# Kernel optimization log

Measured on AMD Instinct MI355X. Metric: run time of the kernel, lower is better.

Reference implementation:

```python
import jax, jax.numpy as jnp
import numpy as np

N, D, NUM_CLASSES = 4096, 512, 128
MARGIN = 0.3


def setup_inputs() -> dict:
    key = jax.random.key(0)
    k1, k2 = jax.random.split(key)
    embeddings = jax.random.normal(k1, (N, D), dtype=jnp.float32)
    labels = jax.random.randint(k2, (N,), 0, NUM_CLASSES, dtype=jnp.int64)
    return {"embeddings": embeddings, "labels": labels}


def _batch_hard_triplet(embeddings, labels, margin):
    # L2-normalize rows (torch F.normalize: x / max(||x||, eps))
    norm = jnp.linalg.norm(embeddings, axis=1, keepdims=True)
    e = embeddings / jnp.maximum(norm, 1e-12)
    n = e.shape[0]
    # Pairwise Euclidean distance via Gram matrix; ||a-b||^2 = 2 - 2 a.b for unit vectors
    gram = e @ e.T                                   # [N, N]
    sq = jnp.clip(2.0 - 2.0 * gram, 0.0, None)
    # safe sqrt: zero (and exactly-equal) pairs get distance 0 with zero gradient
    nz = sq > 0
    dist = jnp.where(nz, jnp.sqrt(jnp.where(nz, sq, 1.0)), 0.0)  # [N, N]

    same = labels[:, None] == labels[None, :]        # [N, N] bool
    eye = jnp.eye(n, dtype=bool)
    pos_mask = same & ~eye                           # positives excluding self
    neg_mask = ~same

    # hardest positive (row max over positives), hardest negative (row min over negatives)
    dist_ap = jnp.max(jnp.where(pos_mask, dist, -jnp.inf), axis=1)  # [N]
    dist_an = jnp.min(jnp.where(neg_mask, dist, jnp.inf), axis=1)   # [N]

    valid = jnp.any(pos_mask, axis=1) & jnp.any(neg_mask, axis=1)   # rows kept by torch loop
    per_row = jax.nn.relu(dist_ap - dist_an + margin)
    num_valid = jnp.sum(valid)
    loss_sum = jnp.sum(jnp.where(valid, per_row, 0.0))
    return jnp.where(num_valid > 0, loss_sum / jnp.maximum(num_valid, 1), 0.0)


def reference(embeddings, labels):
    return _batch_hard_triplet(embeddings, labels, MARGIN)
```

## Files before the change

### kernel.cpp

```cpp
#include <hip/hip_runtime.h>
#include <hip/hip_bf16.h>
#include <stdint.h>


#define NROW 4096
#define DIM  512
#define NCLS 128
#define MARGIN 0.3f
#define BT 128
#define BK 32

typedef __attribute__((ext_vector_type(8))) __bf16 bf16x8;
typedef __attribute__((ext_vector_type(4))) float  f32x4;

__device__ __forceinline__ unsigned enc(float f) {
    unsigned u = __float_as_uint(f);
    return (u & 0x80000000u) ? ~u : (u | 0x80000000u);
}
__device__ __forceinline__ float dec(unsigned e) {
    return (e & 0x80000000u) ? __uint_as_float(e & 0x7fffffffu)
                             : __uint_as_float(~e);
}

__device__ __forceinline__ unsigned short f2bf(float f) {
    __hip_bfloat16 h = __float2bfloat16(f);
    return *reinterpret_cast<unsigned short*>(&h);
}

__device__ __forceinline__ void async_copy16(const void* g, void* l) {
    __builtin_amdgcn_global_load_lds(
        (const __attribute__((address_space(1))) unsigned int*)g,
        (__attribute__((address_space(3))) unsigned int*)l,
        16, 0, 0);
}

__global__ void tl_init(unsigned* __restrict__ posArr, unsigned* __restrict__ negArr,
                        int* __restrict__ cnt) {
    int t = blockIdx.x * blockDim.x + threadIdx.x;
    if (t < NROW) { posArr[t] = 0xFFFFFFFFu; negArr[t] = 0u; }
    if (t < NCLS) cnt[t] = 0;
}

__global__ void tl_norm(const float* __restrict__ E, const int* __restrict__ labels,
                        __hip_bfloat16* __restrict__ Ebf, int* __restrict__ cnt) {
    int wave = threadIdx.x >> 6;
    int lane = threadIdx.x & 63;
    int row  = blockIdx.x * 4 + wave;

    const float4* src = (const float4*)(E + (size_t)row * DIM);
    float4 v0 = src[lane];
    float4 v1 = src[lane + 64];
    float ss = v0.x*v0.x + v0.y*v0.y + v0.z*v0.z + v0.w*v0.w
             + v1.x*v1.x + v1.y*v1.y + v1.z*v1.z + v1.w*v1.w;
    #pragma unroll
    for (int m = 32; m >= 1; m >>= 1) ss += __shfl_xor(ss, m);
    float inv = 1.0f / fmaxf(sqrtf(ss), 1e-12f);

    ushort4 o0, o1;
    o0.x = f2bf(v0.x * inv); o0.y = f2bf(v0.y * inv);
    o0.z = f2bf(v0.z * inv); o0.w = f2bf(v0.w * inv);
    o1.x = f2bf(v1.x * inv); o1.y = f2bf(v1.y * inv);
    o1.z = f2bf(v1.z * inv); o1.w = f2bf(v1.w * inv);
    ushort4* dst = (ushort4*)(Ebf + (size_t)row * DIM);
    dst[lane]      = o0;
    dst[lane + 64] = o1;

    if (lane == 0) atomicAdd(&cnt[labels[row]], 1);
}

__global__ void tl_gram(const __hip_bfloat16* __restrict__ Ebf,
                        const int* __restrict__ labels,
                        unsigned* __restrict__ posArr,
                        unsigned* __restrict__ negArr) {
    __shared__ __align__(16) __hip_bfloat16 At[BT * BK];
    __shared__ __align__(16) __hip_bfloat16 Bt[BT * BK];
    __shared__ int rowLab[BT];
    __shared__ int colLab[BT];

    const int tid  = threadIdx.x;
    const int wave = tid >> 6;
    const int lane = tid & 63;
    const int quad = lane >> 4;
    const int l16  = lane & 15;
    const int wr   = wave >> 1;
    const int wc   = wave & 1;
    const int tileI = blockIdx.y * BT;
    const int tileJ = blockIdx.x * BT;

    if (tid < BT) rowLab[tid] = labels[tileI + tid];
    else          colLab[tid - BT] = labels[tileJ + (tid - BT)];

    const int sRow = wave * 32 + (lane >> 2);
    const int sK   = (lane & 3) * 8;
    const __hip_bfloat16* gA = Ebf + (size_t)(tileI + sRow) * DIM + sK;
    const __hip_bfloat16* gB = Ebf + (size_t)(tileJ + sRow) * DIM + sK;
    __hip_bfloat16* lA0 = &At[(wave * 2 + 0) * 512];
    __hip_bfloat16* lA1 = &At[(wave * 2 + 1) * 512];
    __hip_bfloat16* lB0 = &Bt[(wave * 2 + 0) * 512];
    __hip_bfloat16* lB1 = &Bt[(wave * 2 + 1) * 512];

    f32x4 acc[4][4] = {};

    for (int k0 = 0; k0 < DIM; k0 += BK) {
        async_copy16(gA + k0,            lA0);
        async_copy16(gA + k0 + 16 * DIM, lA1);
        async_copy16(gB + k0,            lB0);
        async_copy16(gB + k0 + 16 * DIM, lB1);
        __syncthreads();

        bf16x8 a[4], b[4];
        #pragma unroll
        for (int mi = 0; mi < 4; mi++)
            a[mi] = *(const bf16x8*)&At[(wr * 64 + mi * 16 + l16) * BK + quad * 8];
        #pragma unroll
        for (int ni = 0; ni < 4; ni++)
            b[ni] = *(const bf16x8*)&Bt[(wc * 64 + ni * 16 + l16) * BK + quad * 8];

        #pragma unroll
        for (int mi = 0; mi < 4; mi++)
            #pragma unroll
            for (int ni = 0; ni < 4; ni++)
                acc[mi][ni] = __builtin_amdgcn_mfma_f32_16x16x32_bf16(
                    a[mi], b[ni], acc[mi][ni], 0, 0, 0);

        __syncthreads();
    }

    #pragma unroll
    for (int mi = 0; mi < 4; mi++) {
        #pragma unroll
        for (int reg = 0; reg < 4; reg++) {
            const int rloc = wr * 64 + mi * 16 + quad * 4 + reg;
            const int lr   = rowLab[rloc];
            const int gi   = tileI + rloc;
            float pmin =  INFINITY;
            float nmax = -INFINITY;
            #pragma unroll
            for (int ni = 0; ni < 4; ni++) {
                const int cloc = wc * 64 + ni * 16 + l16;
                const int gj   = tileJ + cloc;
                const float g  = acc[mi][ni][reg];
                const bool same = (lr == colLab[cloc]);
                if (same && gi != gj) pmin = fminf(pmin, g);
                if (!same)            nmax = fmaxf(nmax, g);
            }
            #pragma unroll
            for (int m = 1; m < 16; m <<= 1) {
                pmin = fminf(pmin, __shfl_xor(pmin, m));
                nmax = fmaxf(nmax, __shfl_xor(nmax, m));
            }
            if (l16 == 0) {
                if (pmin <  INFINITY) atomicMin(&posArr[gi], enc(pmin));
                if (nmax > -INFINITY) atomicMax(&negArr[gi], enc(nmax));
            }
        }
    }
}

__global__ void tl_final(const unsigned* __restrict__ posArr,
                         const unsigned* __restrict__ negArr,
                         const int* __restrict__ labels,
                         const int* __restrict__ cnt,
                         float* __restrict__ out) {
    const int tid = threadIdx.x;
    float sum = 0.0f;
    int   count = 0;
    for (int i = tid; i < NROW; i += 256) {
        const int c = cnt[labels[i]];
        const bool valid = (c >= 2) && (c < NROW);
        const float gp = dec(posArr[i]);
        const float gn = dec(negArr[i]);
        const float dap = sqrtf(fmaxf(2.0f - 2.0f * gp, 0.0f));
        const float dan = sqrtf(fmaxf(2.0f - 2.0f * gn, 0.0f));
        const float per = fmaxf(dap - dan + MARGIN, 0.0f);
        if (valid) { sum += per; count += 1; }
    }
    #pragma unroll
    for (int m = 32; m >= 1; m >>= 1) {
        sum   += __shfl_xor(sum, m);
        count += __shfl_xor(count, m);
    }
    __shared__ float ssum[4];
    __shared__ int   scnt[4];
    const int wave = tid >> 6, lane = tid & 63;
    if (lane == 0) { ssum[wave] = sum; scnt[wave] = count; }
    __syncthreads();
    if (tid == 0) {
        float s = ssum[0] + ssum[1] + ssum[2] + ssum[3];
        int   c = scnt[0] + scnt[1] + scnt[2] + scnt[3];
        out[0] = (c > 0) ? (s / (float)c) : 0.0f;
    }
}

extern "C" void kernel_launch(void* const* d_in, const int* in_sizes, int n_in,
                              void* d_out, int out_size, void* d_ws, size_t ws_size,
                              hipStream_t stream) {
    const float* E      = (const float*)d_in[0];
    const int*   labels = (const int*)d_in[1];
    float*       out    = (float*)d_out;

    char* ws = (char*)d_ws;
    __hip_bfloat16* Ebf   = (__hip_bfloat16*)ws;
    unsigned* posArr      = (unsigned*)(ws + (size_t)NROW * DIM * 2);
    unsigned* negArr      = posArr + NROW;
    int* cnt              = (int*)(negArr + NROW);

    tl_init<<<NROW / 256, 256, 0, stream>>>(posArr, negArr, cnt);
    tl_norm<<<NROW / 4, 256, 0, stream>>>(E, labels, Ebf, cnt);
    dim3 grid(NROW / BT, NROW / BT);
    tl_gram<<<grid, 256, 0, stream>>>(Ebf, labels, posArr, negArr);
    tl_final<<<1, 256, 0, stream>>>(posArr, negArr, labels, cnt, out);
}
```

Baseline: 110.3 us.

## Exploit Gram matrix symmetry by computing only upper-triangular tile pairs

```diff
diff --git a/kernel.cpp b/kernel.cpp
--- a/kernel.cpp
+++ b/kernel.cpp
@@ -5,10 +5,13 @@
 
 #define NROW 4096
 #define DIM  512
-#define NCLS 128
 #define MARGIN 0.3f
 #define BT 128
 #define BK 32
+#define NTILE (NROW / BT)
+#define NPAIR (NTILE * (NTILE + 1) / 2)
+#define POS_INIT 0xFFFFFFFFu
+#define NEG_INIT 0u
 
 typedef __attribute__((ext_vector_type(8))) __bf16 bf16x8;
 typedef __attribute__((ext_vector_type(4))) float  f32x4;
@@ -34,15 +37,15 @@
         16, 0, 0);
 }
 
-__global__ void tl_init(unsigned* __restrict__ posArr, unsigned* __restrict__ negArr,
-                        int* __restrict__ cnt) {
-    int t = blockIdx.x * blockDim.x + threadIdx.x;
-    if (t < NROW) { posArr[t] = 0xFFFFFFFFu; negArr[t] = 0u; }
-    if (t < NCLS) cnt[t] = 0;
-}
-
-__global__ void tl_norm(const float* __restrict__ E, const int* __restrict__ labels,
-                        __hip_bfloat16* __restrict__ Ebf, int* __restrict__ cnt) {
+__global__ void tl_norm(const float* __restrict__ E,
+                        __hip_bfloat16* __restrict__ Ebf,
+                        unsigned* __restrict__ posArr,
+                        unsigned* __restrict__ negArr) {
+    if (blockIdx.x < 16) {
+        int t = blockIdx.x * 256 + threadIdx.x;
+        posArr[t] = POS_INIT;
+        negArr[t] = NEG_INIT;
+    }
     int wave = threadIdx.x >> 6;
     int lane = threadIdx.x & 63;
     int row  = blockIdx.x * 4 + wave;
@@ -64,8 +67,6 @@
     ushort4* dst = (ushort4*)(Ebf + (size_t)row * DIM);
     dst[lane]      = o0;
     dst[lane + 64] = o1;
-
-    if (lane == 0) atomicAdd(&cnt[labels[row]], 1);
 }
 
 __global__ void tl_gram(const __hip_bfloat16* __restrict__ Ebf,
@@ -77,6 +78,10 @@
     __shared__ int rowLab[BT];
     __shared__ int colLab[BT];
 
+    int t = blockIdx.x, bi = 0, rowlen = NTILE;
+    while (t >= rowlen) { t -= rowlen; rowlen--; bi++; }
+    const int bj = bi + t;
+
     const int tid  = threadIdx.x;
     const int wave = tid >> 6;
     const int lane = tid & 63;
@@ -84,8 +89,9 @@
     const int l16  = lane & 15;
     const int wr   = wave >> 1;
     const int wc   = wave & 1;
-    const int tileI = blockIdx.y * BT;
-    const int tileJ = blockIdx.x * BT;
+    const int tileI = bi * BT;
+    const int tileJ = bj * BT;
+    const bool diag = (bi == bj);
 
     if (tid < BT) rowLab[tid] = labels[tileI + tid];
     else          colLab[tid - BT] = labels[tileJ + (tid - BT)];
@@ -126,21 +132,32 @@
         __syncthreads();
     }
 
+    int rl[16], cl[4], clocv[4];
+    #pragma unroll
+    for (int mi = 0; mi < 4; mi++)
+        #pragma unroll
+        for (int reg = 0; reg < 4; reg++)
+            rl[mi * 4 + reg] = rowLab[wr * 64 + mi * 16 + quad * 4 + reg];
+    #pragma unroll
+    for (int ni = 0; ni < 4; ni++) {
+        clocv[ni] = wc * 64 + ni * 16 + l16;
+        cl[ni] = colLab[clocv[ni]];
+    }
+
     #pragma unroll
     for (int mi = 0; mi < 4; mi++) {
         #pragma unroll
         for (int reg = 0; reg < 4; reg++) {
             const int rloc = wr * 64 + mi * 16 + quad * 4 + reg;
-            const int lr   = rowLab[rloc];
+            const int lr   = rl[mi * 4 + reg];
             const int gi   = tileI + rloc;
             float pmin =  INFINITY;
             float nmax = -INFINITY;
             #pragma unroll
             for (int ni = 0; ni < 4; ni++) {
-                const int cloc = wc * 64 + ni * 16 + l16;
-                const int gj   = tileJ + cloc;
-                const float g  = acc[mi][ni][reg];
-                const bool same = (lr == colLab[cloc]);
+                const int gj  = tileJ + clocv[ni];
+                const float g = acc[mi][ni][reg];
+                const bool same = (lr == cl[ni]);
                 if (same && gi != gj) pmin = fminf(pmin, g);
                 if (!same)            nmax = fmaxf(nmax, g);
             }
@@ -155,23 +172,48 @@
             }
         }
     }
+
+    if (!diag) {
+        #pragma unroll
+        for (int ni = 0; ni < 4; ni++) {
+            const int lc = cl[ni];
+            const int gj = tileJ + clocv[ni];
+            float pmin =  INFINITY;
+            float nmax = -INFINITY;
+            #pragma unroll
+            for (int mi = 0; mi < 4; mi++) {
+                #pragma unroll
+                for (int reg = 0; reg < 4; reg++) {
+                    const float g = acc[mi][ni][reg];
+                    const bool same = (rl[mi * 4 + reg] == lc);
+                    if (same) pmin = fminf(pmin, g);
+                    else      nmax = fmaxf(nmax, g);
+                }
+            }
+            pmin = fminf(pmin, __shfl_xor(pmin, 16));
+            pmin = fminf(pmin, __shfl_xor(pmin, 32));
+            nmax = fmaxf(nmax, __shfl_xor(nmax, 16));
+            nmax = fmaxf(nmax, __shfl_xor(nmax, 32));
+            if (quad == 0) {
+                if (pmin <  INFINITY) atomicMin(&posArr[gj], enc(pmin));
+                if (nmax > -INFINITY) atomicMax(&negArr[gj], enc(nmax));
+            }
+        }
+    }
 }
 
 __global__ void tl_final(const unsigned* __restrict__ posArr,
                          const unsigned* __restrict__ negArr,
-                         const int* __restrict__ labels,
-                         const int* __restrict__ cnt,
                          float* __restrict__ out) {
     const int tid = threadIdx.x;
     float sum = 0.0f;
     int   count = 0;
     for (int i = tid; i < NROW; i += 256) {
-        const int c = cnt[labels[i]];
-        const bool valid = (c >= 2) && (c < NROW);
-        const float gp = dec(posArr[i]);
-        const float gn = dec(negArr[i]);
-        const float dap = sqrtf(fmaxf(2.0f - 2.0f * gp, 0.0f));
-        const float dan = sqrtf(fmaxf(2.0f - 2.0f * gn, 0.0f));
+        const unsigned pe = posArr[i];
+        const unsigned ne = negArr[i];
+        const bool valid = (pe != POS_INIT) && (ne != NEG_INIT);
+        const float dap = sqrtf(fmaxf(2.0f - 2.0f * dec(pe), 0.0f));
+        const float dan = sqrtf(fmaxf(2.0f - 2.0f * dec(ne), 0.0f));
         const float per = fmaxf(dap - dan + MARGIN, 0.0f);
         if (valid) { sum += per; count += 1; }
     }
@@ -203,11 +245,8 @@
     __hip_bfloat16* Ebf   = (__hip_bfloat16*)ws;
     unsigned* posArr      = (unsigned*)(ws + (size_t)NROW * DIM * 2);
     unsigned* negArr      = posArr + NROW;
-    int* cnt              = (int*)(negArr + NROW);
-
-    tl_init<<<NROW / 256, 256, 0, stream>>>(posArr, negArr, cnt);
-    tl_norm<<<NROW / 4, 256, 0, stream>>>(E, labels, Ebf, cnt);
-    dim3 grid(NROW / BT, NROW / BT);
-    tl_gram<<<grid, 256, 0, stream>>>(Ebf, labels, posArr, negArr);
-    tl_final<<<1, 256, 0, stream>>>(posArr, negArr, labels, cnt, out);
-}
+
+    tl_norm<<<NROW / 4, 256, 0, stream>>>(E, Ebf, posArr, negArr);
+    tl_gram<<<NPAIR, 256, 0, stream>>>(Ebf, labels, posArr, negArr);
+    tl_final<<<1, 256, 0, stream>>>(posArr, negArr, out);
+}
```

New measurement: 93.43 us. -15.3%, faster.
